# Kernel optimization log

Measured on AMD Instinct MI355X. Metric: run time of the kernel, lower is better.

The kernel has to match this reference:

```python
import jax, jax.numpy as jnp
import numpy as np
import math

N_EMBD = 768
N_HEAD = 8
HEAD_DIM = N_EMBD // N_HEAD


def new_gelu(x):
    c = math.sqrt(2.0 / math.pi)
    return 0.5 * x * (1.0 + jnp.tanh(c * (x + 0.044715 * x * x * x)))


def layer_norm(x, gamma, beta, eps=1e-5):
    mean = jnp.mean(x, axis=-1, keepdims=True)
    var = jnp.maximum(jnp.mean(x * x, axis=-1, keepdims=True) - mean * mean, 0.0)
    return (x - mean) * jax.lax.rsqrt(var + eps) * gamma + beta


def setup_inputs() -> dict:
    key = jax.random.key(0)
    ks = jax.random.split(key, 10)
    C = N_EMBD
    s = lambda n: 1.0 / math.sqrt(n)
    return {
        "x": jax.random.normal(ks[0], (8, 1024, C), dtype=jnp.float32),
        "ln1_g": jnp.ones((C,), jnp.float32),
        "ln1_b": jnp.zeros((C,), jnp.float32),
        "ln2_g": jnp.ones((C,), jnp.float32),
        "ln2_b": jnp.zeros((C,), jnp.float32),
        "W_attn": jax.random.normal(ks[1], (3 * C, C), jnp.float32) * s(C),
        "b_attn": jnp.zeros((3 * C,), jnp.float32),
        "W_proj": jax.random.normal(ks[2], (C, C), jnp.float32) * s(C),
        "b_proj": jnp.zeros((C,), jnp.float32),
        "W_fc": jax.random.normal(ks[3], (4 * C, C), jnp.float32) * s(C),
        "b_fc": jnp.zeros((4 * C,), jnp.float32),
        "W_fc_proj": jax.random.normal(ks[4], (C, 4 * C), jnp.float32) * s(4 * C),
        "b_fc_proj": jnp.zeros((C,), jnp.float32),
    }


def reference(x, ln1_g, ln1_b, ln2_g, ln2_b, W_attn, b_attn, W_proj, b_proj,
              W_fc, b_fc, W_fc_proj, b_fc_proj):
    B, T, C = x.shape
    # --- attention branch ---
    x1 = layer_norm(x, ln1_g, ln1_b)
    qkv = jnp.einsum('btc,oc->bto', x1, W_attn) + b_attn  # [B,T,3C]
    q, k, v = jnp.split(qkv, 3, axis=-1)
    q = q.reshape(B, T, N_HEAD, HEAD_DIM).transpose(0, 2, 1, 3)  # [B,H,T,D]
    k = k.reshape(B, T, N_HEAD, HEAD_DIM).transpose(0, 2, 1, 3)
    v = v.reshape(B, T, N_HEAD, HEAD_DIM).transpose(0, 2, 1, 3)
    att = jnp.einsum('bhqd,bhkd->bhqk', q, k) * (1.0 / math.sqrt(HEAD_DIM))
    causal = jnp.tril(jnp.ones((T, T), bool))
    att = jnp.where(causal[None, None], att, -jnp.inf)
    att = jax.nn.softmax(att, axis=-1)
    y = jnp.einsum('bhqk,bhkd->bhqd', att, v)
    y = y.transpose(0, 2, 1, 3).reshape(B, T, C)
    y = jnp.einsum('btc,oc->bto', y, W_proj) + b_proj
    x = x + y
    # --- MLP branch ---
    x2 = layer_norm(x, ln2_g, ln2_b)
    h = new_gelu(jnp.einsum('btc,oc->bto', x2, W_fc) + b_fc)
    m = jnp.einsum('bth,oh->bto', h, W_fc_proj) + b_fc_proj
    return x + m
```

## Files before the change

kernel.cpp:

```cpp
#include <hip/hip_runtime.h>
#include <math.h>


#define MROWS 8192
#define CDIM  768
#define TSEQ  1024

typedef _Float16 f16x8 __attribute__((ext_vector_type(8)));
typedef _Float16 f16x4 __attribute__((ext_vector_type(4)));
typedef float f32x4 __attribute__((ext_vector_type(4)));

__device__ __forceinline__ void async_copy16(void* lds, const void* g) {
    __builtin_amdgcn_global_load_lds(
        (const __attribute__((address_space(1))) unsigned int*)g,
        (__attribute__((address_space(3))) unsigned int*)lds, 16, 0, 0);
}

__global__ __launch_bounds__(256) void f2h_kernel(const float* __restrict__ in,
                                                  _Float16* __restrict__ out, int n4) {
    int i = blockIdx.x * blockDim.x + threadIdx.x;
    if (i < n4) {
        float4 v = reinterpret_cast<const float4*>(in)[i];
        f16x4 h;
        h[0] = (_Float16)v.x; h[1] = (_Float16)v.y;
        h[2] = (_Float16)v.z; h[3] = (_Float16)v.w;
        reinterpret_cast<f16x4*>(out)[i] = h;
    }
}

__global__ __launch_bounds__(256) void ln_kernel(const float* __restrict__ x,
                                                 const float* __restrict__ g,
                                                 const float* __restrict__ bta,
                                                 _Float16* __restrict__ out) {
    int row = blockIdx.x;
    int t = threadIdx.x;
    const float* xr = x + (size_t)row * CDIM;
    float v0 = xr[t], v1 = xr[t + 256], v2 = xr[t + 512];
    float s = v0 + v1 + v2;
    float q = v0 * v0 + v1 * v1 + v2 * v2;
#pragma unroll
    for (int o = 32; o; o >>= 1) {
        s += __shfl_xor(s, o);
        q += __shfl_xor(q, o);
    }
    __shared__ float ls[4], lq[4];
    int w = t >> 6, lane = t & 63;
    if (lane == 0) { ls[w] = s; lq[w] = q; }
    __syncthreads();
    s = ls[0] + ls[1] + ls[2] + ls[3];
    q = lq[0] + lq[1] + lq[2] + lq[3];
    float mean = s * (1.0f / CDIM);
    float var = fmaxf(q * (1.0f / CDIM) - mean * mean, 0.0f);
    float rstd = rsqrtf(var + 1e-5f);
    _Float16* orow = out + (size_t)row * CDIM;
    orow[t]       = (_Float16)((v0 - mean) * rstd * g[t]       + bta[t]);
    orow[t + 256] = (_Float16)((v1 - mean) * rstd * g[t + 256] + bta[t + 256]);
    orow[t + 512] = (_Float16)((v2 - mean) * rstd * g[t + 512] + bta[t + 512]);
}

template <int EPI, typename OutT>
__global__ __launch_bounds__(256) void hgemm(const _Float16* __restrict__ A,
                                             const _Float16* __restrict__ W,
                                             const float* __restrict__ bias,
                                             const float* __restrict__ res,
                                             OutT* __restrict__ out,
                                             int M, int N, int K) {
    __shared__ _Float16 As[128 * 32];
    __shared__ _Float16 Bs[128 * 32];
    const int t = threadIdx.x;
    const int wid = t >> 6;
    const int l = t & 63;
    const int fr = l & 15;
    const int fq = l >> 4;
    const int wr = wid >> 1, wc = wid & 1;
    const int row0 = blockIdx.y * 128, col0 = blockIdx.x * 128;

    const _Float16* ga = A + (size_t)row0 * K;
    const _Float16* gb = W + (size_t)col0 * K;

    f32x4 acc[4][4] = {};
    const int r_st = t >> 2, c_st = (t & 3) * 8;

    for (int k0 = 0; k0 < K; k0 += 32) {
        __syncthreads();
#pragma unroll
        for (int p = 0; p < 2; ++p) {
            char* la = (char*)As + wid * 1024 + p * 4096;
            char* lb = (char*)Bs + wid * 1024 + p * 4096;
            int r = r_st + p * 64;
            async_copy16(la, ga + (size_t)r * K + k0 + c_st);
            async_copy16(lb, gb + (size_t)r * K + k0 + c_st);
        }
        __syncthreads();

        f16x8 af[4], bf[4];
#pragma unroll
        for (int m = 0; m < 4; ++m)
            af[m] = *reinterpret_cast<const f16x8*>(&As[(wr * 64 + m * 16 + fr) * 32 + fq * 8]);
#pragma unroll
        for (int n = 0; n < 4; ++n)
            bf[n] = *reinterpret_cast<const f16x8*>(&Bs[(wc * 64 + n * 16 + fr) * 32 + fq * 8]);
#pragma unroll
        for (int m = 0; m < 4; ++m)
#pragma unroll
            for (int n = 0; n < 4; ++n)
                acc[m][n] = __builtin_amdgcn_mfma_f32_16x16x32_f16(af[m], bf[n], acc[m][n], 0, 0, 0);
    }

#pragma unroll
    for (int m = 0; m < 4; ++m) {
#pragma unroll
        for (int j = 0; j < 4; ++j) {
            int r = row0 + wr * 64 + m * 16 + fq * 4 + j;
#pragma unroll
            for (int n = 0; n < 4; ++n) {
                int c = col0 + wc * 64 + n * 16 + fr;
                float v = acc[m][n][j] + bias[c];
                if (EPI == 1) v += res[(size_t)r * N + c];
                if (EPI == 2) {
                    float u = v;
                    float inner = 0.7978845608028654f * (u + 0.044715f * u * u * u);
                    v = 0.5f * u * (1.0f + tanhf(inner));
                }
                out[(size_t)r * N + c] = (OutT)v;
            }
        }
    }
}

__global__ __launch_bounds__(256) void attn_kernel(const _Float16* __restrict__ qkv,
                                                   _Float16* __restrict__ y) {
    const int bx = blockIdx.x;
    const int bh = blockIdx.y;
    const int b = bh >> 3, h = bh & 7;
    const int t = threadIdx.x;
    const int wid = t >> 6, l = t & 63;
    const int fr = l & 15, fq = l >> 4;

    __shared__ _Float16 Ks[64 * 104];
    __shared__ _Float16 Vt[96 * 72];
    __shared__ _Float16 Ps[64 * 72];

    const size_t base = (size_t)b * TSEQ * 2304 + h * 96;
    const float scale = 0.10206207261596577f;

    const int kkey = t >> 2, kc = t & 3;
    const int vkey = l, vrow = wid;

    for (int ph = 0; ph < 2; ++ph) {
        const int qt = ph ? (15 - bx) : bx;
        const int q0 = qt * 64;
        const int qrow_g = q0 + wid * 16 + fr;

        f16x8 qa[3];
#pragma unroll
        for (int s = 0; s < 3; ++s)
            qa[s] = *reinterpret_cast<const f16x8*>(
                &qkv[base + (size_t)qrow_g * 2304 + s * 32 + fq * 8]);

        f32x4 O[6] = {};
        float m_i[4], l_i[4];
#pragma unroll
        for (int jj = 0; jj < 4; ++jj) { m_i[jj] = -1e30f; l_i[jj] = 0.0f; }

        f16x8 kreg[3], vreg[3];
#pragma unroll
        for (int p = 0; p < 3; ++p) {
            kreg[p] = *reinterpret_cast<const f16x8*>(
                &qkv[base + (size_t)kkey * 2304 + 768 + 8 * (kc + 4 * p)]);
            vreg[p] = *reinterpret_cast<const f16x8*>(
                &qkv[base + (size_t)vkey * 2304 + 1536 + 8 * (vrow + 4 * p)]);
        }

        for (int kt = 0; kt <= qt; ++kt) {
            __syncthreads();
#pragma unroll
            for (int p = 0; p < 3; ++p)
                *reinterpret_cast<f16x8*>(&Ks[kkey * 104 + 8 * (kc + 4 * p)]) = kreg[p];
#pragma unroll
            for (int p = 0; p < 3; ++p) {
                int dr = 8 * (vrow + 4 * p);
#pragma unroll
                for (int e = 0; e < 8; ++e)
                    Vt[(dr + e) * 72 + vkey] = vreg[p][e];
            }
            __syncthreads();

            if (kt < qt) {
                const int k0n = (kt + 1) * 64;
#pragma unroll
                for (int p = 0; p < 3; ++p) {
                    kreg[p] = *reinterpret_cast<const f16x8*>(
                        &qkv[base + (size_t)(k0n + kkey) * 2304 + 768 + 8 * (kc + 4 * p)]);
                    vreg[p] = *reinterpret_cast<const f16x8*>(
                        &qkv[base + (size_t)(k0n + vkey) * 2304 + 1536 + 8 * (vrow + 4 * p)]);
                }
            }

            f32x4 S[4];
#pragma unroll
            for (int n = 0; n < 4; ++n) {
                f32x4 acc = {};
#pragma unroll
                for (int s = 0; s < 3; ++s) {
                    f16x8 kf = *reinterpret_cast<const f16x8*>(
                        &Ks[(n * 16 + fr) * 104 + s * 32 + fq * 8]);
                    acc = __builtin_amdgcn_mfma_f32_16x16x32_f16(qa[s], kf, acc, 0, 0, 0);
                }
                S[n] = acc;
            }

            const bool diag = (kt == qt);
#pragma unroll
            for (int jj = 0; jj < 4; ++jj) {
                float s0 = S[0][jj] * scale, s1 = S[1][jj] * scale;
                float s2 = S[2][jj] * scale, s3 = S[3][jj] * scale;
                if (diag) {
                    int r = wid * 16 + fq * 4 + jj;
                    if (fr > r)      s0 = -1e30f;
                    if (fr + 16 > r) s1 = -1e30f;
                    if (fr + 32 > r) s2 = -1e30f;
                    if (fr + 48 > r) s3 = -1e30f;
                }
                float mx = fmaxf(fmaxf(s0, s1), fmaxf(s2, s3));
#pragma unroll
                for (int off = 8; off; off >>= 1) mx = fmaxf(mx, __shfl_xor(mx, off, 16));
                float mnew = fmaxf(m_i[jj], mx);
                float sf = __expf(m_i[jj] - mnew);
                m_i[jj] = mnew;
                float p0 = __expf(s0 - mnew), p1 = __expf(s1 - mnew);
                float p2 = __expf(s2 - mnew), p3 = __expf(s3 - mnew);
                float rs = p0 + p1 + p2 + p3;
#pragma unroll
                for (int off = 8; off; off >>= 1) rs += __shfl_xor(rs, off, 16);
                l_i[jj] = l_i[jj] * sf + rs;
                const int prow = wid * 16 + fq * 4 + jj;
                Ps[prow * 72 + fr]      = (_Float16)p0;
                Ps[prow * 72 + 16 + fr] = (_Float16)p1;
                Ps[prow * 72 + 32 + fr] = (_Float16)p2;
                Ps[prow * 72 + 48 + fr] = (_Float16)p3;
#pragma unroll
                for (int n = 0; n < 6; ++n) O[n][jj] *= sf;
            }

#pragma unroll
            for (int ks = 0; ks < 2; ++ks) {
                f16x8 pf = *reinterpret_cast<const f16x8*>(
                    &Ps[(wid * 16 + fr) * 72 + ks * 32 + fq * 8]);
#pragma unroll
                for (int n = 0; n < 6; ++n) {
                    f16x8 vf = *reinterpret_cast<const f16x8*>(
                        &Vt[(n * 16 + fr) * 72 + ks * 32 + fq * 8]);
                    O[n] = __builtin_amdgcn_mfma_f32_16x16x32_f16(pf, vf, O[n], 0, 0, 0);
                }
            }
        }

#pragma unroll
        for (int jj = 0; jj < 4; ++jj) {
            const int q = q0 + wid * 16 + fq * 4 + jj;
            const float invl = 1.0f / l_i[jj];
            _Float16* yr = y + ((size_t)b * TSEQ + q) * CDIM + h * 96;
#pragma unroll
            for (int n = 0; n < 6; ++n)
                yr[n * 16 + fr] = (_Float16)(O[n][jj] * invl);
        }
    }
}

extern "C" void kernel_launch(void* const* d_in, const int* in_sizes, int n_in,
                              void* d_out, int out_size, void* d_ws, size_t ws_size,
                              hipStream_t stream) {
    const float* x        = (const float*)d_in[0];
    const float* ln1_g    = (const float*)d_in[1];
    const float* ln1_b    = (const float*)d_in[2];
    const float* ln2_g    = (const float*)d_in[3];
    const float* ln2_b    = (const float*)d_in[4];
    const float* W_attn   = (const float*)d_in[5];
    const float* b_attn   = (const float*)d_in[6];
    const float* W_proj   = (const float*)d_in[7];
    const float* b_proj   = (const float*)d_in[8];
    const float* W_fc     = (const float*)d_in[9];
    const float* b_fc     = (const float*)d_in[10];
    const float* W_fcproj = (const float*)d_in[11];
    const float* b_fcproj = (const float*)d_in[12];
    float* out = (float*)d_out;

    _Float16* qkvh  = (_Float16*)d_ws;
    _Float16* actsh = qkvh + (size_t)MROWS * 2304;
    _Float16* hh    = actsh + (size_t)MROWS * CDIM;
    _Float16* wah   = hh + (size_t)MROWS * 3072;
    _Float16* wph   = wah + (size_t)2304 * 768;
    _Float16* wfh   = wph + (size_t)768 * 768;
    _Float16* wfph  = wfh + (size_t)3072 * 768;

    dim3 blk(256);

    f2h_kernel<<<dim3((2304 * 768 / 4 + 255) / 256), blk, 0, stream>>>(W_attn, wah, 2304 * 768 / 4);
    f2h_kernel<<<dim3((768 * 768 / 4 + 255) / 256), blk, 0, stream>>>(W_proj, wph, 768 * 768 / 4);
    f2h_kernel<<<dim3((3072 * 768 / 4 + 255) / 256), blk, 0, stream>>>(W_fc, wfh, 3072 * 768 / 4);
    f2h_kernel<<<dim3((768 * 3072 / 4 + 255) / 256), blk, 0, stream>>>(W_fcproj, wfph, 768 * 3072 / 4);

    ln_kernel<<<dim3(MROWS), blk, 0, stream>>>(x, ln1_g, ln1_b, actsh);
    hgemm<0, _Float16><<<dim3(2304 / 128, MROWS / 128), blk, 0, stream>>>(
        actsh, wah, b_attn, nullptr, qkvh, MROWS, 2304, CDIM);
    attn_kernel<<<dim3(8, 64), blk, 0, stream>>>(qkvh, actsh);
    hgemm<1, float><<<dim3(CDIM / 128, MROWS / 128), blk, 0, stream>>>(
        actsh, wph, b_proj, x, out, MROWS, CDIM, CDIM);
    ln_kernel<<<dim3(MROWS), blk, 0, stream>>>(out, ln2_g, ln2_b, actsh);
    hgemm<2, _Float16><<<dim3(3072 / 128, MROWS / 128), blk, 0, stream>>>(
        actsh, wfh, b_fc, nullptr, hh, MROWS, 3072, CDIM);
    hgemm<1, float><<<dim3(CDIM / 128, MROWS / 128), blk, 0, stream>>>(
        hh, wfph, b_fcproj, out, out, MROWS, CDIM, 3072);
}
```

Baseline: 425.2 us.

## Split-K within block for narrow GEMMs and XCD-aware tile swizzle

Adds an hgemm_sk kernel with 512 threads where two groups of four waves each reduce half of K for the same 128x128 tile, then combine partial sums through swizzled LDS before the bias/residual epilogue. It is used for the two N=768 projection GEMMs, whose grid of 384 tiles leaves many CUs lightly occupied. Also remaps block indices so consecutive tiles land on the same XCD, for better L2 reuse across all GEMMs. The cost is an extra LDS reduction pass, more barriers, and larger blocks.

```diff
diff --git a/kernel.cpp b/kernel.cpp
--- a/kernel.cpp
+++ b/kernel.cpp
@@ -14,6 +14,12 @@
     __builtin_amdgcn_global_load_lds(
         (const __attribute__((address_space(1))) unsigned int*)g,
         (__attribute__((address_space(3))) unsigned int*)lds, 16, 0, 0);
+}
+
+__device__ __forceinline__ int xcd_swizzle(int orig, int nwg) {
+    int q = nwg >> 3, r = nwg & 7;
+    int xcd = orig & 7, lid = orig >> 3;
+    return (xcd < r ? xcd * (q + 1) : r * (q + 1) + (xcd - r) * q) + lid;
 }
 
 __global__ __launch_bounds__(256) void f2h_kernel(const float* __restrict__ in,
@@ -73,7 +79,10 @@
     const int fr = l & 15;
     const int fq = l >> 4;
     const int wr = wid >> 1, wc = wid & 1;
-    const int row0 = blockIdx.y * 128, col0 = blockIdx.x * 128;
+
+    const int nx = gridDim.x;
+    const int wg = xcd_swizzle(blockIdx.y * nx + blockIdx.x, nx * gridDim.y);
+    const int row0 = (wg / nx) * 128, col0 = (wg % nx) * 128;
 
     const _Float16* ga = A + (size_t)row0 * K;
     const _Float16* gb = W + (size_t)col0 * K;
@@ -124,6 +133,104 @@
                 }
                 out[(size_t)r * N + c] = (OutT)v;
             }
+        }
+    }
+}
+
+template <int EPI, typename OutT>
+__global__ __launch_bounds__(512) void hgemm_sk(const _Float16* __restrict__ A,
+                                                const _Float16* __restrict__ W,
+                                                const float* __restrict__ bias,
+                                                const float* __restrict__ res,
+                                                OutT* __restrict__ out,
+                                                int M, int N, int K) {
+    __shared__ _Float16 smem[4][128 * 32];
+    const int t = threadIdx.x;
+    const int wid = t >> 6, l = t & 63;
+    const int g = wid >> 2;
+    const int w4 = wid & 3;
+    const int fr = l & 15, fq = l >> 4;
+    const int wr = w4 >> 1, wc = w4 & 1;
+
+    const int nx = gridDim.x;
+    const int wg = xcd_swizzle(blockIdx.y * nx + blockIdx.x, nx * gridDim.y);
+    const int row0 = (wg / nx) * 128, col0 = (wg % nx) * 128;
+
+    const int Khalf = K >> 1;
+    const _Float16* ga = A + (size_t)row0 * K + g * Khalf;
+    const _Float16* gb = W + (size_t)col0 * K + g * Khalf;
+
+    f32x4 acc[4][4] = {};
+    const int tg = w4 * 64 + l;
+    const int r_st = tg >> 2, c_st = (tg & 3) * 8;
+
+    _Float16* As = smem[g];
+    _Float16* Bs = smem[2 + g];
+
+    for (int k0 = 0; k0 < Khalf; k0 += 32) {
+        __syncthreads();
+#pragma unroll
+        for (int p = 0; p < 2; ++p) {
+            char* la = (char*)As + w4 * 1024 + p * 4096;
+            char* lb = (char*)Bs + w4 * 1024 + p * 4096;
+            int r = r_st + p * 64;
+            async_copy16(la, ga + (size_t)r * K + k0 + c_st);
+            async_copy16(lb, gb + (size_t)r * K + k0 + c_st);
+        }
+        __syncthreads();
+
+        f16x8 af[4], bf[4];
+#pragma unroll
+        for (int m = 0; m < 4; ++m)
+            af[m] = *reinterpret_cast<const f16x8*>(&As[(wr * 64 + m * 16 + fr) * 32 + fq * 8]);
+#pragma unroll
+        for (int n = 0; n < 4; ++n)
+            bf[n] = *reinterpret_cast<const f16x8*>(&Bs[(wc * 64 + n * 16 + fr) * 32 + fq * 8]);
+#pragma unroll
+        for (int m = 0; m < 4; ++m)
+#pragma unroll
+            for (int n = 0; n < 4; ++n)
+                acc[m][n] = __builtin_amdgcn_mfma_f32_16x16x32_f16(af[m], bf[n], acc[m][n], 0, 0, 0);
+    }
+
+    float* red = (float*)&smem[0][0];
+#pragma unroll
+    for (int rnd = 0; rnd < 2; ++rnd) {
+        __syncthreads();
+        if (g == 1 && wc == rnd) {
+#pragma unroll
+            for (int m = 0; m < 4; ++m)
+#pragma unroll
+                for (int j = 0; j < 4; ++j) {
+                    int row = wr * 64 + m * 16 + fq * 4 + j;
+                    int sw = (row & 12) << 2;
+#pragma unroll
+                    for (int n = 0; n < 4; ++n)
+                        red[row * 64 + ((n * 16 + fr) ^ sw)] = acc[m][n][j];
+                }
+        }
+        __syncthreads();
+        if (g == 0 && wc == rnd) {
+#pragma unroll
+            for (int m = 0; m < 4; ++m)
+#pragma unroll
+                for (int j = 0; j < 4; ++j) {
+                    int row = wr * 64 + m * 16 + fq * 4 + j;
+                    int sw = (row & 12) << 2;
+                    int r = row0 + row;
+#pragma unroll
+                    for (int n = 0; n < 4; ++n) {
+                        int c = col0 + rnd * 64 + n * 16 + fr;
+                        float v = acc[m][n][j] + red[row * 64 + ((n * 16 + fr) ^ sw)] + bias[c];
+                        if (EPI == 1) v += res[(size_t)r * N + c];
+                        if (EPI == 2) {
+                            float u = v;
+                            float inner = 0.7978845608028654f * (u + 0.044715f * u * u * u);
+                            v = 0.5f * u * (1.0f + tanhf(inner));
+                        }
+                        out[(size_t)r * N + c] = (OutT)v;
+                    }
+                }
         }
     }
 }
@@ -305,11 +412,11 @@
     hgemm<0, _Float16><<<dim3(2304 / 128, MROWS / 128), blk, 0, stream>>>(
         actsh, wah, b_attn, nullptr, qkvh, MROWS, 2304, CDIM);
     attn_kernel<<<dim3(8, 64), blk, 0, stream>>>(qkvh, actsh);
-    hgemm<1, float><<<dim3(CDIM / 128, MROWS / 128), blk, 0, stream>>>(
+    hgemm_sk<1, float><<<dim3(CDIM / 128, MROWS / 128), dim3(512), 0, stream>>>(
         actsh, wph, b_proj, x, out, MROWS, CDIM, CDIM);
     ln_kernel<<<dim3(MROWS), blk, 0, stream>>>(out, ln2_g, ln2_b, actsh);
     hgemm<2, _Float16><<<dim3(3072 / 128, MROWS / 128), blk, 0, stream>>>(
         actsh, wfh, b_fc, nullptr, hh, MROWS, 3072, CDIM);
-    hgemm<1, float><<<dim3(CDIM / 128, MROWS / 128), blk, 0, stream>>>(
+    hgemm_sk<1, float><<<dim3(CDIM / 128, MROWS / 128), dim3(512), 0, stream>>>(
         hh, wfph, b_fcproj, out, out, MROWS, CDIM, 3072);
 }
```

New measurement: 459.2 us. 1.08x slower.

## Add XCD-aware block swizzle, 64-row GEMM for narrow outputs, fuse weight casts

Applied to the files above, without the earlier changes.

Remaps GEMM workgroup IDs so consecutive tiles land on the same XCD, improving L2 reuse of shared A/W panels. Adds a 64x128-tile GEMM variant for the N=768 projections, which doubles the grid from 384 to 768 blocks to better fill the 256 CUs. Merges the four weight f32->f16 conversion launches into one kernel with 4 elements per thread to cut launch overhead. Smaller tiles lower arithmetic intensity per block and the swizzle adds some index arithmetic.

```diff
diff --git a/kernel.cpp b/kernel.cpp
--- a/kernel.cpp
+++ b/kernel.cpp
@@ -16,10 +16,31 @@
         (__attribute__((address_space(3))) unsigned int*)lds, 16, 0, 0);
 }
 
-__global__ __launch_bounds__(256) void f2h_kernel(const float* __restrict__ in,
-                                                  _Float16* __restrict__ out, int n4) {
-    int i = blockIdx.x * blockDim.x + threadIdx.x;
-    if (i < n4) {
+__device__ __forceinline__ int xcd_swizzle(int orig, int nwg) {
+    int q = nwg >> 3, r = nwg & 7;
+    int xcd = orig & 7, lid = orig >> 3;
+    return (xcd < r ? xcd * (q + 1) : r * (q + 1) + (xcd - r) * q) + lid;
+}
+
+__global__ __launch_bounds__(256) void f2h4_kernel(const float* __restrict__ i0,
+                                                   const float* __restrict__ i1,
+                                                   const float* __restrict__ i2,
+                                                   const float* __restrict__ i3,
+                                                   _Float16* __restrict__ o0,
+                                                   _Float16* __restrict__ o1,
+                                                   _Float16* __restrict__ o2,
+                                                   _Float16* __restrict__ o3) {
+    int bb = blockIdx.x;
+    const float* in;
+    _Float16* out;
+    int lb;
+    if (bb < 432)       { in = i0; out = o0; lb = bb; }
+    else if (bb < 576)  { in = i1; out = o1; lb = bb - 432; }
+    else if (bb < 1152) { in = i2; out = o2; lb = bb - 576; }
+    else                { in = i3; out = o3; lb = bb - 1152; }
+    int i = lb * 1024 + threadIdx.x;
+#pragma unroll
+    for (int p = 0; p < 4; ++p, i += 256) {
         float4 v = reinterpret_cast<const float4*>(in)[i];
         f16x4 h;
         h[0] = (_Float16)v.x; h[1] = (_Float16)v.y;
@@ -73,7 +94,10 @@
     const int fr = l & 15;
     const int fq = l >> 4;
     const int wr = wid >> 1, wc = wid & 1;
-    const int row0 = blockIdx.y * 128, col0 = blockIdx.x * 128;
+
+    const int nx = gridDim.x;
+    const int wg = xcd_swizzle(blockIdx.y * nx + blockIdx.x, nx * gridDim.y);
+    const int row0 = (wg / nx) * 128, col0 = (wg % nx) * 128;
 
     const _Float16* ga = A + (size_t)row0 * K;
     const _Float16* gb = W + (size_t)col0 * K;
@@ -112,6 +136,76 @@
 #pragma unroll
         for (int j = 0; j < 4; ++j) {
             int r = row0 + wr * 64 + m * 16 + fq * 4 + j;
+#pragma unroll
+            for (int n = 0; n < 4; ++n) {
+                int c = col0 + wc * 64 + n * 16 + fr;
+                float v = acc[m][n][j] + bias[c];
+                if (EPI == 1) v += res[(size_t)r * N + c];
+                if (EPI == 2) {
+                    float u = v;
+                    float inner = 0.7978845608028654f * (u + 0.044715f * u * u * u);
+                    v = 0.5f * u * (1.0f + tanhf(inner));
+                }
+                out[(size_t)r * N + c] = (OutT)v;
+            }
+        }
+    }
+}
+
+template <int EPI, typename OutT>
+__global__ __launch_bounds__(256) void hgemm64(const _Float16* __restrict__ A,
+                                               const _Float16* __restrict__ W,
+                                               const float* __restrict__ bias,
+                                               const float* __restrict__ res,
+                                               OutT* __restrict__ out,
+                                               int M, int N, int K) {
+    __shared__ _Float16 As[64 * 32];
+    __shared__ _Float16 Bs[128 * 32];
+    const int t = threadIdx.x;
+    const int wid = t >> 6;
+    const int l = t & 63;
+    const int fr = l & 15;
+    const int fq = l >> 4;
+    const int wr = wid >> 1, wc = wid & 1;
+
+    const int nx = gridDim.x;
+    const int wg = xcd_swizzle(blockIdx.y * nx + blockIdx.x, nx * gridDim.y);
+    const int row0 = (wg / nx) * 64, col0 = (wg % nx) * 128;
+
+    const _Float16* ga = A + (size_t)row0 * K;
+    const _Float16* gb = W + (size_t)col0 * K;
+
+    f32x4 acc[2][4] = {};
+    const int rl = l >> 2, cl = (l & 3) * 8;
+
+    for (int k0 = 0; k0 < K; k0 += 32) {
+        __syncthreads();
+        async_copy16((char*)As + wid * 1024, ga + (size_t)(wid * 16 + rl) * K + k0 + cl);
+#pragma unroll
+        for (int p = 0; p < 2; ++p)
+            async_copy16((char*)Bs + wid * 2048 + p * 1024,
+                         gb + (size_t)(wid * 32 + p * 16 + rl) * K + k0 + cl);
+        __syncthreads();
+
+        f16x8 af[2], bf[4];
+#pragma unroll
+        for (int m = 0; m < 2; ++m)
+            af[m] = *reinterpret_cast<const f16x8*>(&As[(wr * 32 + m * 16 + fr) * 32 + fq * 8]);
+#pragma unroll
+        for (int n = 0; n < 4; ++n)
+            bf[n] = *reinterpret_cast<const f16x8*>(&Bs[(wc * 64 + n * 16 + fr) * 32 + fq * 8]);
+#pragma unroll
+        for (int m = 0; m < 2; ++m)
+#pragma unroll
+            for (int n = 0; n < 4; ++n)
+                acc[m][n] = __builtin_amdgcn_mfma_f32_16x16x32_f16(af[m], bf[n], acc[m][n], 0, 0, 0);
+    }
+
+#pragma unroll
+    for (int m = 0; m < 2; ++m) {
+#pragma unroll
+        for (int j = 0; j < 4; ++j) {
+            int r = row0 + wr * 32 + m * 16 + fq * 4 + j;
 #pragma unroll
             for (int n = 0; n < 4; ++n) {
                 int c = col0 + wc * 64 + n * 16 + fr;
@@ -296,20 +390,18 @@
 
     dim3 blk(256);
 
-    f2h_kernel<<<dim3((2304 * 768 / 4 + 255) / 256), blk, 0, stream>>>(W_attn, wah, 2304 * 768 / 4);
-    f2h_kernel<<<dim3((768 * 768 / 4 + 255) / 256), blk, 0, stream>>>(W_proj, wph, 768 * 768 / 4);
-    f2h_kernel<<<dim3((3072 * 768 / 4 + 255) / 256), blk, 0, stream>>>(W_fc, wfh, 3072 * 768 / 4);
-    f2h_kernel<<<dim3((768 * 3072 / 4 + 255) / 256), blk, 0, stream>>>(W_fcproj, wfph, 768 * 3072 / 4);
+    f2h4_kernel<<<dim3(1728), blk, 0, stream>>>(W_attn, W_proj, W_fc, W_fcproj,
+                                                wah, wph, wfh, wfph);
 
     ln_kernel<<<dim3(MROWS), blk, 0, stream>>>(x, ln1_g, ln1_b, actsh);
     hgemm<0, _Float16><<<dim3(2304 / 128, MROWS / 128), blk, 0, stream>>>(
         actsh, wah, b_attn, nullptr, qkvh, MROWS, 2304, CDIM);
     attn_kernel<<<dim3(8, 64), blk, 0, stream>>>(qkvh, actsh);
-    hgemm<1, float><<<dim3(CDIM / 128, MROWS / 128), blk, 0, stream>>>(
+    hgemm64<1, float><<<dim3(CDIM / 128, MROWS / 64), blk, 0, stream>>>(
         actsh, wph, b_proj, x, out, MROWS, CDIM, CDIM);
     ln_kernel<<<dim3(MROWS), blk, 0, stream>>>(out, ln2_g, ln2_b, actsh);
     hgemm<2, _Float16><<<dim3(3072 / 128, MROWS / 128), blk, 0, stream>>>(
         actsh, wfh, b_fc, nullptr, hh, MROWS, 3072, CDIM);
-    hgemm<1, float><<<dim3(CDIM / 128, MROWS / 128), blk, 0, stream>>>(
+    hgemm64<1, float><<<dim3(CDIM / 128, MROWS / 64), blk, 0, stream>>>(
         hh, wfph, b_fcproj, out, out, MROWS, CDIM, 3072);
 }
```

Result: faster. 397.3 us (-6.6%).
